# Kernel tuning notes

Measured on AMD Instinct MI355X. Metric: run time of the kernel, lower is better.

## Reference

```python
import jax, jax.numpy as jnp
import numpy as np

N_USERS, N_ITEMS, N_EDGES, DIM, N_LAYERS = 100000, 50000, 2000000, 64, 3
DECAY = 1e-4
EPS = 1e-12


def setup_inputs() -> dict:
    key = jax.random.key(0)
    ks = jax.random.split(key, 10)
    s_emb = float(np.sqrt(6.0 / (N_USERS + DIM)))  # xavier-ish scale
    return {
        "user_emb": jax.random.normal(ks[0], (N_USERS, DIM), jnp.float32) * 0.05,
        "item_emb": jax.random.normal(ks[1], (N_ITEMS, DIM), jnp.float32) * 0.05,
        # values of the row-normalized (and sparse-dropout-rescaled) adjacency DA
        "edge_val": jax.random.uniform(ks[2], (N_EDGES,), jnp.float32) * 0.1,
        "W": jax.random.normal(ks[3], (N_LAYERS, DIM, DIM), jnp.float32) * float(np.sqrt(1.0 / DIM)),
        "b": jax.random.normal(ks[4], (N_LAYERS, DIM), jnp.float32) * 0.02,
        "edge_row": jax.random.randint(ks[5], (N_EDGES,), 0, N_USERS, jnp.int32),
        "edge_col": jax.random.randint(ks[6], (N_EDGES,), 0, N_ITEMS, jnp.int32),
        "batch_users": jax.random.randint(ks[7], (4096,), 0, N_USERS, jnp.int32),
        "batch_pos": jax.random.randint(ks[8], (4096,), 0, N_ITEMS, jnp.int32),
        "batch_neg": jax.random.randint(ks[9], (4096,), 0, N_ITEMS, jnp.int32),
    }


def _l2_normalize(x):
    n = jnp.sqrt(jnp.sum(x * x, axis=1, keepdims=True))
    return x / jnp.maximum(n, EPS)


def reference(user_emb, item_emb, edge_val, W, b, edge_row, edge_col,
              batch_users, batch_pos, batch_neg):
    n_users, n_items = user_emb.shape[0], item_emb.shape[0]
    # DA @ item_emb  and  DA.T @ user_emb  (layer inputs are always the layer-0
    # embeddings in the original code, so the sparse aggregation is hoisted)
    agg_u = jax.ops.segment_sum(edge_val[:, None] * item_emb[edge_col], edge_row,
                                num_segments=n_users)          # [U, D]
    agg_i = jax.ops.segment_sum(edge_val[:, None] * user_emb[edge_row], edge_col,
                                num_segments=n_items)          # [I, D]
    agg = jnp.concatenate([agg_u, agg_i], axis=0)              # [U+I, D]

    total = [jnp.concatenate([user_emb, item_emb], axis=0)]
    for l in range(W.shape[0]):
        s = agg @ W[l] + b[l]
        s = jax.nn.leaky_relu(s, negative_slope=0.2)
        # message dropout omitted (eval mode / deterministic reference)
        total.append(_l2_normalize(s))
    total = jnp.concatenate(total, axis=1)                     # [U+I, (L+1)*D]

    u_emb_all = total[:n_users]
    i_emb_all = total[n_users:]

    u = u_emb_all[batch_users]
    p = i_emb_all[batch_pos]
    n = i_emb_all[batch_neg]
    pos_scores = jnp.sum(u * p, axis=1)
    neg_scores = jnp.sum(u * n, axis=1)
    mf_loss = -jnp.mean(jax.nn.log_sigmoid(pos_scores - neg_scores))
    regularizer = (jnp.sum(u * u) + jnp.sum(p * p) + jnp.sum(n * n)) / 2.0
    emb_loss = DECAY * regularizer / batch_users.shape[0]
    bpr_loss = mf_loss + emb_loss
    return bpr_loss, u_emb_all, i_emb_all
```

## Files before the change

### kernel.cpp

```cpp
#include <hip/hip_runtime.h>
#include <math.h>

#define N_USERS_C 100000
#define N_ITEMS_C 50000
#define N_NODES_C 150000
#define N_EDGES_C 2000000
#define N_ENTRIES_C 4000000
#define DIM_C 64
#define DECAY_C 1e-4f
#define BATCH_C 4096

#define TILE_EDGES 2048
#define NTILES ((N_EDGES_C + TILE_EDGES - 1) / TILE_EDGES)

#define UB_NODES 391
#define IB_NODES 196
#define NBUCK 512
#define B1_DEPTH 14

#define LOSS_NB (BATCH_C / 4)

#define WS_OFF 0
#define WS_BCNT 150032
#define WS_BSTART 150544
#define WS_CB1 151064
#define WS_ACC 151576
#define WS_WFRAG 151600
#define WS_PART 157744
#define WS_ENT 159792
#define WS_BF16 4159792

#define ENT1_FLOAT_OFF 30400000

typedef __attribute__((ext_vector_type(8))) short short8v;
typedef __attribute__((ext_vector_type(4))) float f32x4;

__device__ __forceinline__ unsigned bf16_bits(float v) {
  unsigned u = __float_as_uint(v);
  return (u + 0x8000u) >> 16;
}

__device__ __forceinline__ short8v as_short8(uint4 u) {
  union { uint4 u4; short8v s8; } x;
  x.u4 = u;
  return x.s8;
}

__global__ __launch_bounds__(256) void cast_kernel(
    const float* __restrict__ user_emb, const float* __restrict__ item_emb,
    ushort* __restrict__ h) {
  const int t = blockIdx.x * 256 + threadIdx.x;
  const int nUser4 = N_USERS_C * DIM_C / 4;
  const int nTot4 = (N_USERS_C + N_ITEMS_C) * DIM_C / 4;
  if (t >= nTot4) return;
  float4 v = (t < nUser4) ? ((const float4*)user_emb)[t]
                          : ((const float4*)item_emb)[t - nUser4];
  ushort4 o;
  o.x = (ushort)bf16_bits(v.x);
  o.y = (ushort)bf16_bits(v.y);
  o.z = (ushort)bf16_bits(v.z);
  o.w = (ushort)bf16_bits(v.w);
  *(ushort4*)&h[(size_t)t * 4] = o;
}

__global__ __launch_bounds__(256) void wprep_kernel(
    const float* __restrict__ W, uint4* __restrict__ wfrag) {
  const int g = blockIdx.x * 256 + threadIdx.x;
  if (g >= 24 * 64) return;
  const int f = g >> 6, l = g & 63;
  const int layer = f >> 3, rem = f & 7, t = rem >> 1, s = rem & 1;
  const int n = t * 16 + (l & 15);
  const int k0 = s * 32 + (l >> 4) * 8;
  const float* base = W + layer * DIM_C * DIM_C + n;
  unsigned r[4];
  #pragma unroll
  for (int j = 0; j < 4; ++j) {
    unsigned lo = bf16_bits(base[(size_t)(k0 + 2 * j) * DIM_C]);
    unsigned hi = bf16_bits(base[(size_t)(k0 + 2 * j + 1) * DIM_C]);
    r[j] = lo | (hi << 16);
  }
  wfrag[g] = make_uint4(r[0], r[1], r[2], r[3]);
}

__global__ __launch_bounds__(256) void bucket_hist_kernel(
    const int* __restrict__ edge_row, const int* __restrict__ edge_col,
    int* __restrict__ bcnt) {
  __shared__ int h[NBUCK];
  const int tid = threadIdx.x;
  for (int i = tid; i < NBUCK; i += 256) h[i] = 0;
  __syncthreads();
  const int base = blockIdx.x * TILE_EDGES;
  #pragma unroll
  for (int k = 0; k < 8; ++k) {
    int e = base + k * 256 + tid;
    if (e < N_EDGES_C) {
      atomicAdd(&h[(int)((unsigned)edge_row[e] / UB_NODES)], 1);
      atomicAdd(&h[256 + (int)((unsigned)edge_col[e] / IB_NODES)], 1);
    }
  }
  __syncthreads();
  for (int i = tid; i < NBUCK; i += 256) {
    int v = h[i];
    if (v) atomicAdd(&bcnt[i], v);
  }
}

__global__ __launch_bounds__(512) void scan512_kernel(
    const int* __restrict__ bcnt, int* __restrict__ bucketStart,
    int* __restrict__ cursB1) {
  __shared__ int ts[512];
  const int t = threadIdx.x;
  int c = bcnt[t];
  ts[t] = c;
  __syncthreads();
  #pragma unroll
  for (int o = 1; o < 512; o <<= 1) {
    int y = (t >= o) ? ts[t - o] : 0;
    __syncthreads();
    ts[t] += y;
    __syncthreads();
  }
  int excl = ts[t] - c;
  bucketStart[t] = excl;
  cursB1[t] = excl;
  if (t == 511) bucketStart[512] = ts[511];
}

__global__ __launch_bounds__(256) void part1_kernel(
    const int* __restrict__ edge_row, const int* __restrict__ edge_col,
    const float* __restrict__ edge_val, int* __restrict__ cursB1,
    int2* __restrict__ ent1) {
  __shared__ int2 stg[NBUCK][B1_DEPTH];
  __shared__ int scnt[NBUCK];
  const int tid = threadIdx.x;
  for (int i = tid; i < NBUCK; i += 256) scnt[i] = 0;
  __syncthreads();

  const int base = blockIdx.x * TILE_EDGES;
  #pragma unroll
  for (int k = 0; k < 8; ++k) {
    int e = base + k * 256 + tid;
    if (e < N_EDGES_C) {
      int r = edge_row[e];
      int c = edge_col[e];
      int vb = __float_as_int(edge_val[e]);
      int ub = (int)((unsigned)r / UB_NODES);
      int2 E1 = make_int2(c | ((r - ub * UB_NODES) << 17), vb);
      int s1 = atomicAdd(&scnt[ub], 1);
      if (s1 < B1_DEPTH) stg[ub][s1] = E1;
      else ent1[atomicAdd(&cursB1[ub], 1)] = E1;
      int ib = (int)((unsigned)c / IB_NODES);
      int2 E2 = make_int2(r | ((c - ib * IB_NODES) << 17), vb);
      ib += 256;
      int s2 = atomicAdd(&scnt[ib], 1);
      if (s2 < B1_DEPTH) stg[ib][s2] = E2;
      else ent1[atomicAdd(&cursB1[ib], 1)] = E2;
    }
  }
  __syncthreads();
  for (int i = tid; i < NBUCK; i += 256) {
    int cn = scnt[i];
    if (cn > B1_DEPTH) cn = B1_DEPTH;
    if (cn) {
      int p = atomicAdd(&cursB1[i], cn);
      for (int j = 0; j < cn; ++j) ent1[p + j] = stg[i][j];
    }
  }
}

__global__ __launch_bounds__(256) void part2_kernel(
    const int* __restrict__ bucketStart, const int2* __restrict__ ent1,
    int* __restrict__ off, unsigned* __restrict__ entP) {
  __shared__ int lhist[512];
  __shared__ int lexcl[512];
  __shared__ int ps[256];
  const int b = blockIdx.x;
  const int tid = threadIdx.x;
  int nb, nodes;
  if (b < 256) {
    nb = b * UB_NODES;
    int e = (b + 1) * UB_NODES;
    if (e > N_USERS_C) e = N_USERS_C;
    nodes = e - nb;
  } else {
    nb = N_USERS_C + (b - 256) * IB_NODES;
    int e = N_USERS_C + (b - 255) * IB_NODES;
    if (e > N_NODES_C) e = N_NODES_C;
    nodes = e - nb;
  }
  const int start = bucketStart[b];
  const int end = bucketStart[b + 1];

  for (int i = tid; i < 512; i += 256) lhist[i] = 0;
  __syncthreads();

  for (int i = start + tid; i < end; i += 256)
    atomicAdd(&lhist[(unsigned)ent1[i].x >> 17], 1);
  __syncthreads();

  int a0 = lhist[2 * tid];
  int a1 = lhist[2 * tid + 1];
  ps[tid] = a0 + a1;
  __syncthreads();
  #pragma unroll
  for (int o = 1; o < 256; o <<= 1) {
    int y = (tid >= o) ? ps[tid - o] : 0;
    __syncthreads();
    ps[tid] += y;
    __syncthreads();
  }
  int e0 = ps[tid] - a0 - a1;
  lexcl[2 * tid] = e0;
  lexcl[2 * tid + 1] = e0 + a0;
  __syncthreads();

  for (int t = tid; t < nodes; t += 256) off[nb + t] = start + lexcl[t];
  if (b == NBUCK - 1 && tid == 0) off[N_NODES_C] = N_ENTRIES_C;

  for (int i = tid; i < 512; i += 256) lhist[i] = lexcl[i];
  __syncthreads();

  const bool isUser = (b < 256);
  for (int i = start + tid; i < end; i += 256) {
    int2 E = ent1[i];
    int local = (int)((unsigned)E.x >> 17);
    int src = E.x & 0x1FFFF;
    unsigned hb = bf16_bits(__int_as_float(E.y));
    unsigned P;
    if (isUser) {
      P = (hb << 16) | (unsigned)src;
    } else {
      P = (((hb & 0xFFFEu) | ((unsigned)src & 1u)) << 16) |
          ((unsigned)src >> 1);
    }
    int p = start + atomicAdd(&lhist[local], 1);
    entP[p] = P;
  }
}

__device__ __forceinline__ void acc_row8(float* __restrict__ a, unsigned E,
                                         bool isUser,
                                         const ushort* __restrict__ tblU,
                                         const ushort* __restrict__ tblI,
                                         int ol) {
  unsigned src;
  float v;
  const ushort* t;
  if (isUser) {
    src = E & 0xFFFFu;
    v = __uint_as_float(E & 0xFFFF0000u);
    t = tblI;
  } else {
    src = ((E & 0xFFFFu) << 1) | ((E >> 16) & 1u);
    v = __uint_as_float(E & 0xFFFE0000u);
    t = tblU;
  }
  uint4 q = *(const uint4*)(t + ((size_t)src << 6) + (ol << 3));
  a[0] += v * __uint_as_float(q.x << 16);
  a[1] += v * __uint_as_float(q.x & 0xFFFF0000u);
  a[2] += v * __uint_as_float(q.y << 16);
  a[3] += v * __uint_as_float(q.y & 0xFFFF0000u);
  a[4] += v * __uint_as_float(q.z << 16);
  a[5] += v * __uint_as_float(q.z & 0xFFFF0000u);
  a[6] += v * __uint_as_float(q.w << 16);
  a[7] += v * __uint_as_float(q.w & 0xFFFF0000u);
}

__global__ __launch_bounds__(256) void gather_kernel(
    const ushort* __restrict__ bf16tab, const int* __restrict__ off,
    const unsigned* __restrict__ entP, float* __restrict__ out) {
  const int lane = threadIdx.x & 63;
  const int og = lane >> 3;
  const int ol = lane & 7;
  const int wave0 = (blockIdx.x * 256 + threadIdx.x) >> 6;
  const int nWaves = gridDim.x * 4;
  const ushort* tblU = bf16tab;
  const ushort* tblI = bf16tab + (size_t)N_USERS_C * DIM_C;

  for (int n = wave0; n < N_NODES_C; n += nWaves) {
    const bool isUser = (n < N_USERS_C);
    int i = off[n] + og;
    const int end = off[n + 1];
    float a[8] = {0.f, 0.f, 0.f, 0.f, 0.f, 0.f, 0.f, 0.f};
    for (; i + 8 < end; i += 16) {
      unsigned E0 = entP[i];
      unsigned E1 = entP[i + 8];
      acc_row8(a, E0, isUser, tblU, tblI, ol);
      acc_row8(a, E1, isUser, tblU, tblI, ol);
    }
    if (i < end) acc_row8(a, entP[i], isUser, tblU, tblI, ol);

    #pragma unroll
    for (int k = 0; k < 8; ++k) {
      a[k] += __shfl_xor(a[k], 8);
      a[k] += __shfl_xor(a[k], 16);
      a[k] += __shfl_xor(a[k], 32);
    }
    if (lane < 8) {
      uint4 o;
      o.x = bf16_bits(a[0]) | (bf16_bits(a[1]) << 16);
      o.y = bf16_bits(a[2]) | (bf16_bits(a[3]) << 16);
      o.z = bf16_bits(a[4]) | (bf16_bits(a[5]) << 16);
      o.w = bf16_bits(a[6]) | (bf16_bits(a[7]) << 16);
      ((uint4*)(out + 4 + (size_t)n * 256))[ol] = o;
    }
  }
}

__global__ __launch_bounds__(256) void transform_kernel(
    const float* __restrict__ user_emb, const float* __restrict__ item_emb,
    const uint4* __restrict__ wfragG, const float* __restrict__ bvec,
    float* __restrict__ out) {
  __shared__ uint4 Wf[24 * 64];
  const int tid = threadIdx.x;
  for (int i = tid; i < 24 * 64; i += 256) Wf[i] = wfragG[i];
  __syncthreads();

  const int wave = tid >> 6;
  const int lane = tid & 63;
  const int nb = blockIdx.x * 64 + wave * 16;
  if (nb >= N_NODES_C) return;
  const int q = lane >> 4;
  const int col = lane & 15;

  const uint4* aggp = (const uint4*)(out + 4 + (size_t)(nb + col) * 256);
  short8v A0 = as_short8(aggp[q]);
  short8v A1 = as_short8(aggp[q + 4]);

  for (int l = 0; l < 3; ++l) {
    f32x4 c[4];
    #pragma unroll
    for (int t = 0; t < 4; ++t) c[t] = (f32x4){0.f, 0.f, 0.f, 0.f};
    const uint4* wl = &Wf[l * 8 * 64];
    #pragma unroll
    for (int t = 0; t < 4; ++t) {
      c[t] = __builtin_amdgcn_mfma_f32_16x16x32_bf16(
          A0, as_short8(wl[(t * 2 + 0) * 64 + lane]), c[t], 0, 0, 0);
      c[t] = __builtin_amdgcn_mfma_f32_16x16x32_bf16(
          A1, as_short8(wl[(t * 2 + 1) * 64 + lane]), c[t], 0, 0, 0);
    }

    float sq[4] = {0.f, 0.f, 0.f, 0.f};
    #pragma unroll
    for (int t = 0; t < 4; ++t) {
      const float bt = bvec[l * DIM_C + t * 16 + col];
      #pragma unroll
      for (int r = 0; r < 4; ++r) {
        float v = c[t][r] + bt;
        v = (v >= 0.f) ? v : 0.2f * v;
        c[t][r] = v;
        sq[r] += v * v;
      }
    }
    #pragma unroll
    for (int r = 0; r < 4; ++r) {
      #pragma unroll
      for (int m = 1; m < 16; m <<= 1) sq[r] += __shfl_xor(sq[r], m);
      sq[r] = 1.0f / fmaxf(sqrtf(sq[r]), 1e-12f);
    }
    #pragma unroll
    for (int t = 0; t < 4; ++t) {
      #pragma unroll
      for (int r = 0; r < 4; ++r) {
        const int node = nb + q * 4 + r;
        out[1 + (size_t)node * 256 + (size_t)(l + 1) * 64 + t * 16 + col] =
            c[t][r] * sq[r];
      }
    }
  }

  for (int idx = lane; idx < 16 * DIM_C; idx += 64) {
    const int node = nb + (idx >> 6);
    const int cc = idx & 63;
    float e = (node < N_USERS_C)
                  ? user_emb[(size_t)node * DIM_C + cc]
                  : item_emb[(size_t)(node - N_USERS_C) * DIM_C + cc];
    out[1 + (size_t)node * 256 + cc] = e;
  }
}

__global__ __launch_bounds__(256) void loss_kernel(
    const float* __restrict__ out, const int* __restrict__ bu,
    const int* __restrict__ bp, const int* __restrict__ bn,
    float* __restrict__ part) {
  __shared__ float smf[4];
  __shared__ float srg[4];
  const int wave = threadIdx.x >> 6;
  const int lane = threadIdx.x & 63;
  const int j = blockIdx.x * 4 + wave;

  const float* urow = out + 1 + (size_t)bu[j] * 256;
  const float* prow = out + 1 + ((size_t)N_USERS_C + bp[j]) * 256;
  const float* nrow = out + 1 + ((size_t)N_USERS_C + bn[j]) * 256;

  float4 u = ((const float4*)urow)[lane];
  float4 pp = ((const float4*)prow)[lane];
  float4 nn = ((const float4*)nrow)[lane];

  float x = u.x * (pp.x - nn.x) + u.y * (pp.y - nn.y) +
            u.z * (pp.z - nn.z) + u.w * (pp.w - nn.w);
  float r = u.x * u.x + u.y * u.y + u.z * u.z + u.w * u.w +
            pp.x * pp.x + pp.y * pp.y + pp.z * pp.z + pp.w * pp.w +
            nn.x * nn.x + nn.y * nn.y + nn.z * nn.z + nn.w * nn.w;

  #pragma unroll
  for (int o = 32; o; o >>= 1) {
    x += __shfl_xor(x, o);
    r += __shfl_xor(r, o);
  }
  if (lane == 0) {
    float ls = fminf(x, 0.f) - log1pf(expf(-fabsf(x)));
    smf[wave] = -ls;
    srg[wave] = 0.5f * r;
  }
  __syncthreads();
  if (threadIdx.x == 0) {
    part[blockIdx.x] = smf[0] + smf[1] + smf[2] + smf[3];
    part[LOSS_NB + blockIdx.x] = srg[0] + srg[1] + srg[2] + srg[3];
  }
}

__global__ __launch_bounds__(256) void finalize_kernel(
    const float* __restrict__ part, float* __restrict__ out) {
  __shared__ float smf[4];
  __shared__ float srg[4];
  const int tid = threadIdx.x;
  float mf = 0.f, rg = 0.f;
  #pragma unroll
  for (int k = 0; k < LOSS_NB / 256; ++k) {
    mf += part[tid + k * 256];
    rg += part[LOSS_NB + tid + k * 256];
  }
  #pragma unroll
  for (int o = 32; o; o >>= 1) {
    mf += __shfl_xor(mf, o);
    rg += __shfl_xor(rg, o);
  }
  if ((tid & 63) == 0) {
    smf[tid >> 6] = mf;
    srg[tid >> 6] = rg;
  }
  __syncthreads();
  if (tid == 0) {
    float m = smf[0] + smf[1] + smf[2] + smf[3];
    float g = srg[0] + srg[1] + srg[2] + srg[3];
    out[0] = m / (float)BATCH_C + DECAY_C * g / (float)BATCH_C;
  }
}

extern "C" void kernel_launch(void* const* d_in, const int* in_sizes, int n_in,
                              void* d_out, int out_size, void* d_ws, size_t ws_size,
                              hipStream_t stream) {
  const float* user_emb = (const float*)d_in[0];
  const float* item_emb = (const float*)d_in[1];
  const float* edge_val = (const float*)d_in[2];
  const float* W        = (const float*)d_in[3];
  const float* bvec     = (const float*)d_in[4];
  const int* edge_row   = (const int*)d_in[5];
  const int* edge_col   = (const int*)d_in[6];
  const int* bu         = (const int*)d_in[7];
  const int* bp         = (const int*)d_in[8];
  const int* bn         = (const int*)d_in[9];

  float* out = (float*)d_out;
  int* ws = (int*)d_ws;
  int* off         = ws + WS_OFF;
  int* bcnt        = ws + WS_BCNT;
  int* bucketStart = ws + WS_BSTART;
  int* cursB1      = ws + WS_CB1;
  uint4* wfrag     = (uint4*)(ws + WS_WFRAG);
  float* part      = (float*)(ws + WS_PART);
  unsigned* entP   = (unsigned*)(ws + WS_ENT);
  ushort* bf16tab  = (ushort*)(ws + WS_BF16);
  int2* ent1       = (int2*)(out + ENT1_FLOAT_OFF);

  hipMemsetAsync(bcnt, 0, NBUCK * sizeof(int), stream);

  cast_kernel<<<(2400000 + 255) / 256, 256, 0, stream>>>(user_emb, item_emb,
                                                         bf16tab);
  wprep_kernel<<<6, 256, 0, stream>>>(W, wfrag);
  bucket_hist_kernel<<<NTILES, 256, 0, stream>>>(edge_row, edge_col, bcnt);
  scan512_kernel<<<1, 512, 0, stream>>>(bcnt, bucketStart, cursB1);
  part1_kernel<<<NTILES, 256, 0, stream>>>(edge_row, edge_col, edge_val,
                                           cursB1, ent1);
  part2_kernel<<<NBUCK, 256, 0, stream>>>(bucketStart, ent1, off, entP);
  gather_kernel<<<2048, 256, 0, stream>>>(bf16tab, off, entP, out);
  transform_kernel<<<(N_NODES_C + 63) / 64, 256, 0, stream>>>(
      user_emb, item_emb, wfrag, bvec, out);
  loss_kernel<<<LOSS_NB, 256, 0, stream>>>(out, bu, bp, bn, part);
  finalize_kernel<<<1, 256, 0, stream>>>(part, out);
}
```

Baseline: 286.6 us.

## Fuse prep kernels, gather+transform, loss+finalize; compact partition entries

Merges the cast, weight-fragment prep and bucket histogram into one launch. Part1 now emits a packed 32-bit payload plus a 16-bit local index, replacing 8-byte entries, so part2 moves fewer bytes. The gather and transform kernels become one kernel that keeps aggregates in shared memory instead of writing them to the output and reading them back. Loss and finalize are joined using a last-block atomic counter. This cuts launches and global memory traffic, at the cost of fixed 16-node-per-wave gather work, which may balance load less evenly than the old grid-stride loop.

```diff
diff --git a/kernel.cpp b/kernel.cpp
--- a/kernel.cpp
+++ b/kernel.cpp
@@ -12,6 +12,7 @@
 
 #define TILE_EDGES 2048
 #define NTILES ((N_EDGES_C + TILE_EDGES - 1) / TILE_EDGES)
+#define CAST_NB 9375
 
 #define UB_NODES 391
 #define IB_NODES 196
@@ -19,18 +20,20 @@
 #define B1_DEPTH 14
 
 #define LOSS_NB (BATCH_C / 4)
+#define NGROUP 9375
 
 #define WS_OFF 0
 #define WS_BCNT 150032
 #define WS_BSTART 150544
 #define WS_CB1 151064
-#define WS_ACC 151576
+#define WS_CTR 151576
 #define WS_WFRAG 151600
 #define WS_PART 157744
 #define WS_ENT 159792
 #define WS_BF16 4159792
 
-#define ENT1_FLOAT_OFF 30400000
+#define ENT1P_FLOAT_OFF 30400000
+#define ENT1N_FLOAT_OFF 34400000
 
 typedef __attribute__((ext_vector_type(8))) short short8v;
 typedef __attribute__((ext_vector_type(4))) float f32x4;
@@ -46,62 +49,61 @@
   return x.s8;
 }
 
-__global__ __launch_bounds__(256) void cast_kernel(
+__global__ __launch_bounds__(256) void prep_kernel(
     const float* __restrict__ user_emb, const float* __restrict__ item_emb,
-    ushort* __restrict__ h) {
-  const int t = blockIdx.x * 256 + threadIdx.x;
-  const int nUser4 = N_USERS_C * DIM_C / 4;
-  const int nTot4 = (N_USERS_C + N_ITEMS_C) * DIM_C / 4;
-  if (t >= nTot4) return;
-  float4 v = (t < nUser4) ? ((const float4*)user_emb)[t]
-                          : ((const float4*)item_emb)[t - nUser4];
-  ushort4 o;
-  o.x = (ushort)bf16_bits(v.x);
-  o.y = (ushort)bf16_bits(v.y);
-  o.z = (ushort)bf16_bits(v.z);
-  o.w = (ushort)bf16_bits(v.w);
-  *(ushort4*)&h[(size_t)t * 4] = o;
-}
-
-__global__ __launch_bounds__(256) void wprep_kernel(
-    const float* __restrict__ W, uint4* __restrict__ wfrag) {
-  const int g = blockIdx.x * 256 + threadIdx.x;
-  if (g >= 24 * 64) return;
-  const int f = g >> 6, l = g & 63;
-  const int layer = f >> 3, rem = f & 7, t = rem >> 1, s = rem & 1;
-  const int n = t * 16 + (l & 15);
-  const int k0 = s * 32 + (l >> 4) * 8;
-  const float* base = W + layer * DIM_C * DIM_C + n;
-  unsigned r[4];
-  #pragma unroll
-  for (int j = 0; j < 4; ++j) {
-    unsigned lo = bf16_bits(base[(size_t)(k0 + 2 * j) * DIM_C]);
-    unsigned hi = bf16_bits(base[(size_t)(k0 + 2 * j + 1) * DIM_C]);
-    r[j] = lo | (hi << 16);
-  }
-  wfrag[g] = make_uint4(r[0], r[1], r[2], r[3]);
-}
-
-__global__ __launch_bounds__(256) void bucket_hist_kernel(
-    const int* __restrict__ edge_row, const int* __restrict__ edge_col,
-    int* __restrict__ bcnt) {
-  __shared__ int h[NBUCK];
+    const float* __restrict__ W, const int* __restrict__ edge_row,
+    const int* __restrict__ edge_col, ushort* __restrict__ h,
+    uint4* __restrict__ wfrag, int* __restrict__ bcnt) {
+  __shared__ int hist[NBUCK];
+  const int b = blockIdx.x;
   const int tid = threadIdx.x;
-  for (int i = tid; i < NBUCK; i += 256) h[i] = 0;
-  __syncthreads();
-  const int base = blockIdx.x * TILE_EDGES;
-  #pragma unroll
-  for (int k = 0; k < 8; ++k) {
-    int e = base + k * 256 + tid;
-    if (e < N_EDGES_C) {
-      atomicAdd(&h[(int)((unsigned)edge_row[e] / UB_NODES)], 1);
-      atomicAdd(&h[256 + (int)((unsigned)edge_col[e] / IB_NODES)], 1);
-    }
-  }
-  __syncthreads();
-  for (int i = tid; i < NBUCK; i += 256) {
-    int v = h[i];
-    if (v) atomicAdd(&bcnt[i], v);
+
+  if (b < CAST_NB) {
+    const int t = b * 256 + tid;
+    const int nUser4 = N_USERS_C * DIM_C / 4;
+    const int nTot4 = (N_USERS_C + N_ITEMS_C) * DIM_C / 4;
+    if (t >= nTot4) return;
+    float4 v = (t < nUser4) ? ((const float4*)user_emb)[t]
+                            : ((const float4*)item_emb)[t - nUser4];
+    ushort4 o;
+    o.x = (ushort)bf16_bits(v.x);
+    o.y = (ushort)bf16_bits(v.y);
+    o.z = (ushort)bf16_bits(v.z);
+    o.w = (ushort)bf16_bits(v.w);
+    *(ushort4*)&h[(size_t)t * 4] = o;
+  } else if (b < CAST_NB + 6) {
+    const int g = (b - CAST_NB) * 256 + tid;
+    if (g >= 24 * 64) return;
+    const int f = g >> 6, l = g & 63;
+    const int layer = f >> 3, rem = f & 7, t = rem >> 1, s = rem & 1;
+    const int n = t * 16 + (l & 15);
+    const int k0 = s * 32 + (l >> 4) * 8;
+    const float* base = W + layer * DIM_C * DIM_C + n;
+    unsigned r[4];
+    #pragma unroll
+    for (int j = 0; j < 4; ++j) {
+      unsigned lo = bf16_bits(base[(size_t)(k0 + 2 * j) * DIM_C]);
+      unsigned hi = bf16_bits(base[(size_t)(k0 + 2 * j + 1) * DIM_C]);
+      r[j] = lo | (hi << 16);
+    }
+    wfrag[g] = make_uint4(r[0], r[1], r[2], r[3]);
+  } else {
+    for (int i = tid; i < NBUCK; i += 256) hist[i] = 0;
+    __syncthreads();
+    const int base = (b - CAST_NB - 6) * TILE_EDGES;
+    #pragma unroll
+    for (int k = 0; k < 8; ++k) {
+      int e = base + k * 256 + tid;
+      if (e < N_EDGES_C) {
+        atomicAdd(&hist[(int)((unsigned)edge_row[e] / UB_NODES)], 1);
+        atomicAdd(&hist[256 + (int)((unsigned)edge_col[e] / IB_NODES)], 1);
+      }
+    }
+    __syncthreads();
+    for (int i = tid; i < NBUCK; i += 256) {
+      int v = hist[i];
+      if (v) atomicAdd(&bcnt[i], v);
+    }
   }
 }
 
@@ -129,8 +131,9 @@
 __global__ __launch_bounds__(256) void part1_kernel(
     const int* __restrict__ edge_row, const int* __restrict__ edge_col,
     const float* __restrict__ edge_val, int* __restrict__ cursB1,
-    int2* __restrict__ ent1) {
-  __shared__ int2 stg[NBUCK][B1_DEPTH];
+    ushort* __restrict__ ent1N, unsigned* __restrict__ ent1P) {
+  __shared__ unsigned stgP[NBUCK][B1_DEPTH];
+  __shared__ ushort stgN[NBUCK][B1_DEPTH];
   __shared__ int scnt[NBUCK];
   const int tid = threadIdx.x;
   for (int i = tid; i < NBUCK; i += 256) scnt[i] = 0;
@@ -143,18 +146,33 @@
     if (e < N_EDGES_C) {
       int r = edge_row[e];
       int c = edge_col[e];
-      int vb = __float_as_int(edge_val[e]);
+      unsigned hb = bf16_bits(edge_val[e]);
       int ub = (int)((unsigned)r / UB_NODES);
-      int2 E1 = make_int2(c | ((r - ub * UB_NODES) << 17), vb);
+      ushort loc1 = (ushort)(r - ub * UB_NODES);
+      unsigned P1 = (hb << 16) | (unsigned)c;
       int s1 = atomicAdd(&scnt[ub], 1);
-      if (s1 < B1_DEPTH) stg[ub][s1] = E1;
-      else ent1[atomicAdd(&cursB1[ub], 1)] = E1;
+      if (s1 < B1_DEPTH) {
+        stgP[ub][s1] = P1;
+        stgN[ub][s1] = loc1;
+      } else {
+        int p = atomicAdd(&cursB1[ub], 1);
+        ent1P[p] = P1;
+        ent1N[p] = loc1;
+      }
       int ib = (int)((unsigned)c / IB_NODES);
-      int2 E2 = make_int2(r | ((c - ib * IB_NODES) << 17), vb);
-      ib += 256;
-      int s2 = atomicAdd(&scnt[ib], 1);
-      if (s2 < B1_DEPTH) stg[ib][s2] = E2;
-      else ent1[atomicAdd(&cursB1[ib], 1)] = E2;
+      ushort loc2 = (ushort)(c - ib * IB_NODES);
+      unsigned P2 = (((hb & 0xFFFEu) | ((unsigned)r & 1u)) << 16) |
+                    ((unsigned)r >> 1);
+      int b2 = 256 + ib;
+      int s2 = atomicAdd(&scnt[b2], 1);
+      if (s2 < B1_DEPTH) {
+        stgP[b2][s2] = P2;
+        stgN[b2][s2] = loc2;
+      } else {
+        int p = atomicAdd(&cursB1[b2], 1);
+        ent1P[p] = P2;
+        ent1N[p] = loc2;
+      }
     }
   }
   __syncthreads();
@@ -163,14 +181,18 @@
     if (cn > B1_DEPTH) cn = B1_DEPTH;
     if (cn) {
       int p = atomicAdd(&cursB1[i], cn);
-      for (int j = 0; j < cn; ++j) ent1[p + j] = stg[i][j];
+      for (int j = 0; j < cn; ++j) {
+        ent1P[p + j] = stgP[i][j];
+        ent1N[p + j] = stgN[i][j];
+      }
     }
   }
 }
 
 __global__ __launch_bounds__(256) void part2_kernel(
-    const int* __restrict__ bucketStart, const int2* __restrict__ ent1,
-    int* __restrict__ off, unsigned* __restrict__ entP) {
+    const int* __restrict__ bucketStart, const ushort* __restrict__ ent1N,
+    const unsigned* __restrict__ ent1P, int* __restrict__ off,
+    unsigned* __restrict__ entP) {
   __shared__ int lhist[512];
   __shared__ int lexcl[512];
   __shared__ int ps[256];
@@ -195,7 +217,7 @@
   __syncthreads();
 
   for (int i = start + tid; i < end; i += 256)
-    atomicAdd(&lhist[(unsigned)ent1[i].x >> 17], 1);
+    atomicAdd(&lhist[ent1N[i]], 1);
   __syncthreads();
 
   int a0 = lhist[2 * tid];
@@ -220,21 +242,10 @@
   for (int i = tid; i < 512; i += 256) lhist[i] = lexcl[i];
   __syncthreads();
 
-  const bool isUser = (b < 256);
   for (int i = start + tid; i < end; i += 256) {
-    int2 E = ent1[i];
-    int local = (int)((unsigned)E.x >> 17);
-    int src = E.x & 0x1FFFF;
-    unsigned hb = bf16_bits(__int_as_float(E.y));
-    unsigned P;
-    if (isUser) {
-      P = (hb << 16) | (unsigned)src;
-    } else {
-      P = (((hb & 0xFFFEu) | ((unsigned)src & 1u)) << 16) |
-          ((unsigned)src >> 1);
-    }
+    int local = ent1N[i];
     int p = start + atomicAdd(&lhist[local], 1);
-    entP[p] = P;
+    entP[p] = ent1P[i];
   }
 }
 
@@ -266,66 +277,66 @@
   a[7] += v * __uint_as_float(q.w & 0xFFFF0000u);
 }
 
-__global__ __launch_bounds__(256) void gather_kernel(
+__global__ __launch_bounds__(256) void fused_gt_kernel(
     const ushort* __restrict__ bf16tab, const int* __restrict__ off,
-    const unsigned* __restrict__ entP, float* __restrict__ out) {
-  const int lane = threadIdx.x & 63;
+    const unsigned* __restrict__ entP, const float* __restrict__ user_emb,
+    const float* __restrict__ item_emb, const uint4* __restrict__ wfragG,
+    const float* __restrict__ bvec, float* __restrict__ out) {
+  __shared__ uint4 Wf[24 * 64];
+  __shared__ uint4 aggS[4 * 144];
+  const int tid = threadIdx.x;
+  for (int i = tid; i < 24 * 64; i += 256) Wf[i] = wfragG[i];
+
+  const int wave = tid >> 6;
+  const int lane = tid & 63;
   const int og = lane >> 3;
   const int ol = lane & 7;
-  const int wave0 = (blockIdx.x * 256 + threadIdx.x) >> 6;
-  const int nWaves = gridDim.x * 4;
+  const int g = blockIdx.x * 4 + wave;
+  const bool active = (g < NGROUP);
+  const int nb = g * 16;
+  uint4* __restrict__ myAgg = &aggS[wave * 144];
   const ushort* tblU = bf16tab;
   const ushort* tblI = bf16tab + (size_t)N_USERS_C * DIM_C;
 
-  for (int n = wave0; n < N_NODES_C; n += nWaves) {
-    const bool isUser = (n < N_USERS_C);
-    int i = off[n] + og;
-    const int end = off[n + 1];
-    float a[8] = {0.f, 0.f, 0.f, 0.f, 0.f, 0.f, 0.f, 0.f};
-    for (; i + 8 < end; i += 16) {
-      unsigned E0 = entP[i];
-      unsigned E1 = entP[i + 8];
-      acc_row8(a, E0, isUser, tblU, tblI, ol);
-      acc_row8(a, E1, isUser, tblU, tblI, ol);
-    }
-    if (i < end) acc_row8(a, entP[i], isUser, tblU, tblI, ol);
-
-    #pragma unroll
-    for (int k = 0; k < 8; ++k) {
-      a[k] += __shfl_xor(a[k], 8);
-      a[k] += __shfl_xor(a[k], 16);
-      a[k] += __shfl_xor(a[k], 32);
-    }
-    if (lane < 8) {
-      uint4 o;
-      o.x = bf16_bits(a[0]) | (bf16_bits(a[1]) << 16);
-      o.y = bf16_bits(a[2]) | (bf16_bits(a[3]) << 16);
-      o.z = bf16_bits(a[4]) | (bf16_bits(a[5]) << 16);
-      o.w = bf16_bits(a[6]) | (bf16_bits(a[7]) << 16);
-      ((uint4*)(out + 4 + (size_t)n * 256))[ol] = o;
-    }
-  }
-}
-
-__global__ __launch_bounds__(256) void transform_kernel(
-    const float* __restrict__ user_emb, const float* __restrict__ item_emb,
-    const uint4* __restrict__ wfragG, const float* __restrict__ bvec,
-    float* __restrict__ out) {
-  __shared__ uint4 Wf[24 * 64];
-  const int tid = threadIdx.x;
-  for (int i = tid; i < 24 * 64; i += 256) Wf[i] = wfragG[i];
-  __syncthreads();
-
-  const int wave = tid >> 6;
-  const int lane = tid & 63;
-  const int nb = blockIdx.x * 64 + wave * 16;
-  if (nb >= N_NODES_C) return;
+  if (active) {
+    #pragma unroll 1
+    for (int j = 0; j < 16; ++j) {
+      const int n = nb + j;
+      const bool isUser = (n < N_USERS_C);
+      int i = off[n] + og;
+      const int end = off[n + 1];
+      float a[8] = {0.f, 0.f, 0.f, 0.f, 0.f, 0.f, 0.f, 0.f};
+      for (; i + 8 < end; i += 16) {
+        unsigned E0 = entP[i];
+        unsigned E1 = entP[i + 8];
+        acc_row8(a, E0, isUser, tblU, tblI, ol);
+        acc_row8(a, E1, isUser, tblU, tblI, ol);
+      }
+      if (i < end) acc_row8(a, entP[i], isUser, tblU, tblI, ol);
+
+      #pragma unroll
+      for (int k = 0; k < 8; ++k) {
+        a[k] += __shfl_xor(a[k], 8);
+        a[k] += __shfl_xor(a[k], 16);
+        a[k] += __shfl_xor(a[k], 32);
+      }
+      if (lane < 8) {
+        uint4 o;
+        o.x = bf16_bits(a[0]) | (bf16_bits(a[1]) << 16);
+        o.y = bf16_bits(a[2]) | (bf16_bits(a[3]) << 16);
+        o.z = bf16_bits(a[4]) | (bf16_bits(a[5]) << 16);
+        o.w = bf16_bits(a[6]) | (bf16_bits(a[7]) << 16);
+        myAgg[j * 9 + ol] = o;
+      }
+    }
+  }
+  __syncthreads();
+  if (!active) return;
+
   const int q = lane >> 4;
   const int col = lane & 15;
-
-  const uint4* aggp = (const uint4*)(out + 4 + (size_t)(nb + col) * 256);
-  short8v A0 = as_short8(aggp[q]);
-  short8v A1 = as_short8(aggp[q + 4]);
+  short8v A0 = as_short8(myAgg[col * 9 + q]);
+  short8v A1 = as_short8(myAgg[col * 9 + q + 4]);
 
   for (int l = 0; l < 3; ++l) {
     f32x4 c[4];
@@ -380,18 +391,20 @@
 }
 
 __global__ __launch_bounds__(256) void loss_kernel(
-    const float* __restrict__ out, const int* __restrict__ bu,
+    const float* __restrict__ out_ro, const int* __restrict__ bu,
     const int* __restrict__ bp, const int* __restrict__ bn,
-    float* __restrict__ part) {
+    float* __restrict__ part, int* __restrict__ ctr,
+    float* __restrict__ out) {
   __shared__ float smf[4];
   __shared__ float srg[4];
+  __shared__ bool isLast;
   const int wave = threadIdx.x >> 6;
   const int lane = threadIdx.x & 63;
   const int j = blockIdx.x * 4 + wave;
 
-  const float* urow = out + 1 + (size_t)bu[j] * 256;
-  const float* prow = out + 1 + ((size_t)N_USERS_C + bp[j]) * 256;
-  const float* nrow = out + 1 + ((size_t)N_USERS_C + bn[j]) * 256;
+  const float* urow = out_ro + 1 + (size_t)bu[j] * 256;
+  const float* prow = out_ro + 1 + ((size_t)N_USERS_C + bp[j]) * 256;
+  const float* nrow = out_ro + 1 + ((size_t)N_USERS_C + bn[j]) * 256;
 
   float4 u = ((const float4*)urow)[lane];
   float4 pp = ((const float4*)prow)[lane];
@@ -417,13 +430,13 @@
   if (threadIdx.x == 0) {
     part[blockIdx.x] = smf[0] + smf[1] + smf[2] + smf[3];
     part[LOSS_NB + blockIdx.x] = srg[0] + srg[1] + srg[2] + srg[3];
-  }
-}
-
-__global__ __launch_bounds__(256) void finalize_kernel(
-    const float* __restrict__ part, float* __restrict__ out) {
-  __shared__ float smf[4];
-  __shared__ float srg[4];
+    __threadfence();
+    isLast = (atomicAdd(ctr, 1) == LOSS_NB - 1);
+  }
+  __syncthreads();
+  if (!isLast) return;
+  __threadfence();
+
   const int tid = threadIdx.x;
   float mf = 0.f, rg = 0.f;
   #pragma unroll
@@ -436,9 +449,9 @@
     mf += __shfl_xor(mf, o);
     rg += __shfl_xor(rg, o);
   }
-  if ((tid & 63) == 0) {
-    smf[tid >> 6] = mf;
-    srg[tid >> 6] = rg;
+  if (lane == 0) {
+    smf[wave] = mf;
+    srg[wave] = rg;
   }
   __syncthreads();
   if (tid == 0) {
@@ -468,25 +481,23 @@
   int* bcnt        = ws + WS_BCNT;
   int* bucketStart = ws + WS_BSTART;
   int* cursB1      = ws + WS_CB1;
+  int* lossCtr     = ws + WS_CTR;
   uint4* wfrag     = (uint4*)(ws + WS_WFRAG);
   float* part      = (float*)(ws + WS_PART);
   unsigned* entP   = (unsigned*)(ws + WS_ENT);
   ushort* bf16tab  = (ushort*)(ws + WS_BF16);
-  int2* ent1       = (int2*)(out + ENT1_FLOAT_OFF);
-
-  hipMemsetAsync(bcnt, 0, NBUCK * sizeof(int), stream);
-
-  cast_kernel<<<(2400000 + 255) / 256, 256, 0, stream>>>(user_emb, item_emb,
-                                                         bf16tab);
-  wprep_kernel<<<6, 256, 0, stream>>>(W, wfrag);
-  bucket_hist_kernel<<<NTILES, 256, 0, stream>>>(edge_row, edge_col, bcnt);
+  unsigned* ent1P  = (unsigned*)(out + ENT1P_FLOAT_OFF);
+  ushort* ent1N    = (ushort*)(out + ENT1N_FLOAT_OFF);
+
+  hipMemsetAsync(bcnt, 0, (size_t)(WS_CTR + 16 - WS_BCNT) * sizeof(int), stream);
+
+  prep_kernel<<<CAST_NB + 6 + NTILES, 256, 0, stream>>>(
+      user_emb, item_emb, W, edge_row, edge_col, bf16tab, wfrag, bcnt);
   scan512_kernel<<<1, 512, 0, stream>>>(bcnt, bucketStart, cursB1);
   part1_kernel<<<NTILES, 256, 0, stream>>>(edge_row, edge_col, edge_val,
-                                           cursB1, ent1);
-  part2_kernel<<<NBUCK, 256, 0, stream>>>(bucketStart, ent1, off, entP);
-  gather_kernel<<<2048, 256, 0, stream>>>(bf16tab, off, entP, out);
-  transform_kernel<<<(N_NODES_C + 63) / 64, 256, 0, stream>>>(
-      user_emb, item_emb, wfrag, bvec, out);
-  loss_kernel<<<LOSS_NB, 256, 0, stream>>>(out, bu, bp, bn, part);
-  finalize_kernel<<<1, 256, 0, stream>>>(part, out);
-}
+                                           cursB1, ent1N, ent1P);
+  part2_kernel<<<NBUCK, 256, 0, stream>>>(bucketStart, ent1N, ent1P, off, entP);
+  fused_gt_kernel<<<(NGROUP + 3) / 4, 256, 0, stream>>>(
+      bf16tab, off, entP, user_emb, item_emb, wfrag, bvec, out);
+  loss_kernel<<<LOSS_NB, 256, 0, stream>>>(out, bu, bp, bn, part, lossCtr, out);
+}
```

After: 339.7 us. 1.19x slower.
